# Performance work log

Hardware: AMD Instinct MI355X
Metric: run time of the kernel (lower is better)

The kernel has to match this reference:

```python
import jax, jax.numpy as jnp
import numpy as np

B, S, D = 2, 2048, 2048
H, KV, HD = 32, 8, 64  # num_heads, num_kv_heads, head_dim
NREP = H // KV


def rotate_half(x):
    x1, x2 = x[..., : x.shape[-1] // 2], x[..., x.shape[-1] // 2 :]
    return jnp.concatenate((-x2, x1), axis=-1)


def setup_inputs() -> dict:
    key = jax.random.key(0)
    ks = jax.random.split(key, 5)
    x = jax.random.normal(ks[0], (B, S, D), dtype=jnp.float32)
    # weights stored as [in, out] so y = x @ W (same math as nn.Linear with random init)
    Wq = jax.random.normal(ks[1], (D, D), dtype=jnp.float32) * (D ** -0.5)
    Wk = jax.random.normal(ks[2], (D, KV * HD), dtype=jnp.float32) * (D ** -0.5)
    Wv = jax.random.normal(ks[3], (D, KV * HD), dtype=jnp.float32) * (D ** -0.5)
    Wo = jax.random.normal(ks[4], (D, D), dtype=jnp.float32) * (D ** -0.5)
    # standard RoPE tables, broadcastable over [B, H, S, HD]
    inv_freq = 1.0 / (10000.0 ** (jnp.arange(0, HD, 2, dtype=jnp.float32) / HD))
    freqs = jnp.arange(S, dtype=jnp.float32)[:, None] * inv_freq[None, :]  # [S, HD/2]
    emb = jnp.concatenate((freqs, freqs), axis=-1)  # [S, HD]
    cos = jnp.cos(emb)[None, None]  # [1,1,S,HD]
    sin = jnp.sin(emb)[None, None]
    # causal mask, masked where == 0
    attention_mask = jnp.tril(jnp.ones((S, S), dtype=jnp.int32))[None, None]
    return {"x": x, "cos": cos, "sin": sin, "Wq": Wq, "Wk": Wk, "Wv": Wv,
            "Wo": Wo, "attention_mask": attention_mask}


def reference(x, cos, sin, Wq, Wk, Wv, Wo, attention_mask):
    b, s, _ = x.shape
    q = (x @ Wq).reshape(b, s, H, HD).transpose(0, 2, 1, 3)   # [B,H,S,HD]
    k = (x @ Wk).reshape(b, s, KV, HD).transpose(0, 2, 1, 3)  # [B,KV,S,HD]
    v = (x @ Wv).reshape(b, s, KV, HD).transpose(0, 2, 1, 3)  # [B,KV,S,HD]
    # RoPE (elementwise) commutes with head-repeat; apply before grouping
    q = q * cos + rotate_half(q) * sin
    k = k * cos + rotate_half(k) * sin
    # GQA head broadcast instead of repeat_interleave: group q as [B,KV,NREP,S,HD]
    qg = q.reshape(b, KV, NREP, s, HD)
    scores = jnp.einsum('bgrqd,bgkd->bgrqk', qg, k) / jnp.sqrt(jnp.float32(HD))
    scores = jnp.where(attention_mask[:, :, None] == 0, jnp.float32(-1e9), scores)
    probs = jax.nn.softmax(scores, axis=-1)
    out = jnp.einsum('bgrqk,bgkd->bgrqd', probs, v)           # [B,KV,NREP,S,HD]
    out = out.reshape(b, H, s, HD).transpose(0, 2, 1, 3).reshape(b, s, H * HD)
    return out @ Wo
```

## Files before the change

### kernel.cpp

```cpp
#include <hip/hip_runtime.h>
#include <hip/hip_bf16.h>
#include <stdint.h>

#define B_ 2
#define S_ 2048
#define D_ 2048
#define H_ 32
#define KV_ 8
#define HD_ 64
#define NQKV 3072

typedef __bf16 bf16_t;
typedef __bf16 bf16x8 __attribute__((ext_vector_type(8)));
typedef __bf16 bf16x4 __attribute__((ext_vector_type(4)));
typedef float  f32x4  __attribute__((ext_vector_type(4)));
typedef float  f32x16 __attribute__((ext_vector_type(16)));
typedef unsigned int u32;
typedef u32 u32x4 __attribute__((ext_vector_type(4)));

typedef const __attribute__((address_space(1))) uint32_t* gp1_t;
typedef __attribute__((address_space(3))) uint32_t* lp3_t;

__device__ inline void gload_lds16(const void* g, void* l) {
  __builtin_amdgcn_global_load_lds((gp1_t)(uintptr_t)g, (lp3_t)(uint32_t)(uintptr_t)l,
                                   16, 0, 0);
}

__device__ inline u32 pkbf(float a, float b) {
  union { bf16_t h[2]; u32 u; } v;
  v.h[0] = (bf16_t)a; v.h[1] = (bf16_t)b;
  return v.u;
}

__device__ inline void pl32swap(u32 &a, u32 &b) {
  asm("v_permlane32_swap_b32 %0, %1" : "+v"(a), "+v"(b));
}

__global__ void prep_all(const float* __restrict__ x, bf16_t* __restrict__ xb,
                         const float* __restrict__ Wq, const float* __restrict__ Wk,
                         const float* __restrict__ Wv, const float* __restrict__ Wo,
                         bf16_t* __restrict__ Wqkvt, bf16_t* __restrict__ Wot) {
  const int id = blockIdx.x;
  const int tid = threadIdx.y * 32 + threadIdx.x;
  if (id < 8192) {
    const int i = id * 256 + tid;
    float4 v = ((const float4*)x)[i];
    bf16x4 o;
    o[0] = (bf16_t)v.x; o[1] = (bf16_t)v.y; o[2] = (bf16_t)v.z; o[3] = (bf16_t)v.w;
    ((bf16x4*)xb)[i] = o;
    return;
  }
  __shared__ float t[32][33];
  const int wid = id - 8192;
  const float* in; bf16_t* out; int C, roff, bx, by;
  if (wid < 4096)      { in = Wq; out = Wqkvt; C = 2048; roff = 0;    bx = wid & 63;          by = wid >> 6; }
  else if (wid < 5120) { in = Wk; out = Wqkvt; C = 512;  roff = 2048; bx = (wid - 4096) & 15; by = (wid - 4096) >> 4; }
  else if (wid < 6144) { in = Wv; out = Wqkvt; C = 512;  roff = 2560; bx = (wid - 5120) & 15; by = (wid - 5120) >> 4; }
  else                 { in = Wo; out = Wot;   C = 2048; roff = 0;    bx = (wid - 6144) & 63; by = (wid - 6144) >> 6; }
  const int tx = threadIdx.x, ty = threadIdx.y;
  const int c0 = bx * 32, r0 = by * 32;
#pragma unroll
  for (int j = 0; j < 4; ++j)
    t[ty + j*8][tx] = in[(int64_t)(r0 + ty + j*8) * C + c0 + tx];
  __syncthreads();
#pragma unroll
  for (int j = 0; j < 4; ++j)
    out[(int64_t)(roff + c0 + ty + j*8) * 2048 + r0 + tx] = (bf16_t)t[tx][ty + j*8];
}

__global__ void v_transpose(const bf16_t* __restrict__ qkv, bf16_t* __restrict__ Vt) {
  __shared__ bf16_t t[32][34];
  const int tx = threadIdx.x, ty = threadIdx.y;
  const int c0 = blockIdx.x * 32;
  const int s0 = blockIdx.y * 32;
  const int b  = blockIdx.z;
#pragma unroll
  for (int j = 0; j < 4; ++j)
    t[ty + j*8][tx] = qkv[(int64_t)(b * S_ + s0 + ty + j*8) * NQKV + 2560 + c0 + tx];
  __syncthreads();
#pragma unroll
  for (int j = 0; j < 4; ++j)
    Vt[(int64_t)(b * 512 + c0 + ty + j*8) * S_ + s0 + tx] = t[tx][ty + j*8];
}

#define QSCALE 0.18033688011112042f
__global__ __launch_bounds__(256) void rope_scatter2(const bf16_t* __restrict__ qkv,
                                                     const float* __restrict__ cosb,
                                                     const float* __restrict__ sinb,
                                                     bf16_t* __restrict__ Q,
                                                     bf16_t* __restrict__ Kr) {
  const int row = blockIdx.x;
  const int b = row >> 11, s = row & 2047;
  const bf16_t* src = qkv + (int64_t)row * NQKV;
  const float* cs = cosb + s * HD_;
  const float* sn = sinb + s * HD_;
  const int tid = threadIdx.x;
  {
    const int c0 = tid * 8;
    const int d0 = c0 & 63, h = c0 >> 6;
    bf16x8 own = *(const bf16x8*)(src + c0);
    bf16x8 par = *(const bf16x8*)(src + (c0 ^ 32));
    const float sgn = (d0 & 32) ? 1.f : -1.f;
    bf16x8 o;
#pragma unroll
    for (int j = 0; j < 8; ++j) {
      const int d = d0 + j;
      float val = (float)own[j] * cs[d] + sgn * (float)par[j] * sn[d];
      o[j] = (bf16_t)(val * QSCALE);
    }
    *(bf16x8*)(Q + ((int64_t)(b * H_ + h) * S_ + s) * HD_ + d0) = o;
  }
  if (tid < 64) {
    const int c0 = 2048 + tid * 8;
    const int d0 = (tid * 8) & 63, kvh = tid >> 3;
    bf16x8 own = *(const bf16x8*)(src + c0);
    bf16x8 par = *(const bf16x8*)(src + (c0 ^ 32));
    const float sgn = (d0 & 32) ? 1.f : -1.f;
    bf16x8 o;
#pragma unroll
    for (int j = 0; j < 8; ++j) {
      const int d = d0 + j;
      float val = (float)own[j] * cs[d] + sgn * (float)par[j] * sn[d];
      o[j] = (bf16_t)val;
    }
    *(bf16x8*)(Kr + ((int64_t)(b * KV_ + kvh) * S_ + s) * HD_ + d0) = o;
  }
}

template <int BN, int EPI, typename OutT>
__global__ __launch_bounds__(512, 2) void gemm256(const bf16_t* __restrict__ A,
                                                  const bf16_t* __restrict__ Bt,
                                                  OutT* __restrict__ Cout,
                                                  int N, int K) {
  constexpr int NB = BN / 64;
  constexpr int LT = 4 + NB;
  constexpr int WCOLS = BN / 4;
  constexpr int NF = WCOLS / 16;

  __shared__ bf16_t As[2][256 * 64];
  __shared__ bf16_t Bs[2][BN * 64];

  const int tid = threadIdx.x;
  const int w = tid >> 6, lane = tid & 63;
  const int l15 = lane & 15, l4 = lane >> 4;
  const int wr = w >> 2, wc = w & 3;

  const int nX = gridDim.x;
  const int lin = blockIdx.y * nX + blockIdx.x;
  const int cpx = (nX * gridDim.y) >> 3;
  const int swz = (lin & 7) * cpx + (lin >> 3);
  const int bm = (swz / nX) * 256, bn = (swz % nX) * BN;

  const int rw = w * 8 + (lane >> 3);
  const int srcg = ((lane & 7) ^ ((lane >> 3) & 7)) << 3;
  const bf16_t* PA[4];
  const bf16_t* PB[NB];
#pragma unroll
  for (int L = 0; L < 4; ++L)
    PA[L] = A + (int64_t)(bm + L * 64 + rw) * K + srcg;
#pragma unroll
  for (int L = 0; L < NB; ++L)
    PB[L] = Bt + (int64_t)(bn + L * 64 + rw) * K + srcg;

  const int NK = K >> 6;
  const int xr = l15 & 7;
  const int g0 = (l4 ^ xr) << 3;
  const int g1 = ((4 + l4) ^ xr) << 3;

  f32x4 acc[8][NF] = {};

  auto stage = [&](int s, int buf, int toff) {
    if (s < 4) gload_lds16(PA[s] + toff, &As[buf][s * 4096 + w * 512]);
    else       gload_lds16(PB[s - 4] + toff, &Bs[buf][(s - 4) * 4096 + w * 512]);
  };

#pragma unroll
  for (int s = 0; s < LT; ++s) stage(s, 0, 0);
  asm volatile("s_waitcnt vmcnt(0)" ::: "memory");
  __syncthreads();

  for (int t = 0; t < NK; ++t) {
    const int p = t & 1;
    const bool more = (t + 1) < NK;
    const int toff = (t + 1) << 6;
    const bf16_t* Ab = &As[p][0];
    const bf16_t* Bb = &Bs[p][0];

    bf16x8 ball[NF][2];
#pragma unroll
    for (int nn = 0; nn < NF; ++nn) {
      const int rb = wc * WCOLS + nn * 16 + l15;
      ball[nn][0] = *(const bf16x8*)(Bb + rb * 64 + g0);
      ball[nn][1] = *(const bf16x8*)(Bb + rb * 64 + g1);
    }

#pragma unroll
    for (int mh = 0; mh < 2; ++mh) {
      if (more) {
        const int sb = mh * (LT / 2);
        const int se = (mh == 0) ? (LT / 2) : LT;
#pragma unroll
        for (int s = sb; s < se; ++s) stage(s, p ^ 1, toff);
      }
      bf16x8 af[4][2];
#pragma unroll
      for (int mm = 0; mm < 4; ++mm) {
        const int ra = wr * 128 + (mh * 4 + mm) * 16 + l15;
        af[mm][0] = *(const bf16x8*)(Ab + ra * 64 + g0);
        af[mm][1] = *(const bf16x8*)(Ab + ra * 64 + g1);
      }
      __builtin_amdgcn_s_setprio(1);
#pragma unroll
      for (int mm = 0; mm < 4; ++mm)
#pragma unroll
        for (int nn = 0; nn < NF; ++nn) {
          acc[mh*4+mm][nn] = __builtin_amdgcn_mfma_f32_16x16x32_bf16(
              af[mm][0], ball[nn][0], acc[mh*4+mm][nn], 0, 0, 0);
          acc[mh*4+mm][nn] = __builtin_amdgcn_mfma_f32_16x16x32_bf16(
              af[mm][1], ball[nn][1], acc[mh*4+mm][nn], 0, 0, 0);
        }
      __builtin_amdgcn_s_setprio(0);
    }
    if (more) {
      asm volatile("s_waitcnt vmcnt(0)" ::: "memory");
      __syncthreads();
    }
  }

#pragma unroll
  for (int m = 0; m < 8; ++m) {
    const int row = bm + wr * 128 + m * 16 + l4 * 4;
#pragma unroll
    for (int n = 0; n < NF; ++n) {
      const int col = bn + wc * WCOLS + n * 16 + l15;
#pragma unroll
      for (int r = 0; r < 4; ++r)
        Cout[(int64_t)(row + r) * N + col] = (OutT)acc[m][n][r];
    }
  }
}

__global__ __launch_bounds__(512, 2) void gemm_out3(const bf16_t* __restrict__ A,
                                                    const bf16_t* __restrict__ Bt,
                                                    float* __restrict__ Cout,
                                                    int N, int K) {
  constexpr int BN = 128, NB = 2, LT = 6, WCOLS = 32, NF = 2;

  __shared__ bf16_t As[3][256 * 64];
  __shared__ bf16_t Bs[3][BN * 64];

  const int tid = threadIdx.x;
  const int w = tid >> 6, lane = tid & 63;
  const int l15 = lane & 15, l4 = lane >> 4;
  const int wr = w >> 2, wc = w & 3;

  const int nX = gridDim.x;
  const int lin = blockIdx.y * nX + blockIdx.x;
  const int cpx = (nX * gridDim.y) >> 3;
  const int swz = (lin & 7) * cpx + (lin >> 3);
  const int bm = (swz / nX) * 256, bn = (swz % nX) * BN;

  const int rw = w * 8 + (lane >> 3);
  const int srcg = ((lane & 7) ^ ((lane >> 3) & 7)) << 3;
  const bf16_t* PA[4];
  const bf16_t* PB[NB];
#pragma unroll
  for (int L = 0; L < 4; ++L)
    PA[L] = A + (int64_t)(bm + L * 64 + rw) * K + srcg;
#pragma unroll
  for (int L = 0; L < NB; ++L)
    PB[L] = Bt + (int64_t)(bn + L * 64 + rw) * K + srcg;

  const int NK = K >> 6;
  const int xr = l15 & 7;
  const int g0 = (l4 ^ xr) << 3;
  const int g1 = ((4 + l4) ^ xr) << 3;

  f32x4 acc[8][NF] = {};

  auto stage = [&](int tsrc, int buf) {
    const int tc = (tsrc < NK) ? tsrc : (NK - 1);
    const int toff = tc << 6;
#pragma unroll
    for (int s = 0; s < 4; ++s)
      gload_lds16(PA[s] + toff, &As[buf][s * 4096 + w * 512]);
#pragma unroll
    for (int s = 0; s < NB; ++s)
      gload_lds16(PB[s] + toff, &Bs[buf][s * 4096 + w * 512]);
  };

  stage(0, 0);
  stage(1, 1);

  for (int t = 0; t < NK; ++t) {
    asm volatile("s_waitcnt vmcnt(6)" ::: "memory");
    asm volatile("s_barrier" ::: "memory");
    stage(t + 2, (t + 2) % 3);
    const bf16_t* Ab = &As[t % 3][0];
    const bf16_t* Bb = &Bs[t % 3][0];

    bf16x8 ball[NF][2];
#pragma unroll
    for (int nn = 0; nn < NF; ++nn) {
      const int rb = wc * WCOLS + nn * 16 + l15;
      ball[nn][0] = *(const bf16x8*)(Bb + rb * 64 + g0);
      ball[nn][1] = *(const bf16x8*)(Bb + rb * 64 + g1);
    }
#pragma unroll
    for (int mh = 0; mh < 2; ++mh) {
      bf16x8 af[4][2];
#pragma unroll
      for (int mm = 0; mm < 4; ++mm) {
        const int ra = wr * 128 + (mh * 4 + mm) * 16 + l15;
        af[mm][0] = *(const bf16x8*)(Ab + ra * 64 + g0);
        af[mm][1] = *(const bf16x8*)(Ab + ra * 64 + g1);
      }
      __builtin_amdgcn_s_setprio(1);
#pragma unroll
      for (int mm = 0; mm < 4; ++mm)
#pragma unroll
        for (int nn = 0; nn < NF; ++nn) {
          acc[mh*4+mm][nn] = __builtin_amdgcn_mfma_f32_16x16x32_bf16(
              af[mm][0], ball[nn][0], acc[mh*4+mm][nn], 0, 0, 0);
          acc[mh*4+mm][nn] = __builtin_amdgcn_mfma_f32_16x16x32_bf16(
              af[mm][1], ball[nn][1], acc[mh*4+mm][nn], 0, 0, 0);
        }
      __builtin_amdgcn_s_setprio(0);
    }
  }
  asm volatile("s_waitcnt vmcnt(0)" ::: "memory");

#pragma unroll
  for (int m = 0; m < 8; ++m) {
    const int row = bm + wr * 128 + m * 16 + l4 * 4;
#pragma unroll
    for (int n = 0; n < NF; ++n) {
      const int col = bn + wc * WCOLS + n * 16 + l15;
#pragma unroll
      for (int r = 0; r < 4; ++r)
        Cout[(int64_t)(row + r) * N + col] = acc[m][n][r];
    }
  }
}

#define SHIFT_ 8.0f
__global__ __launch_bounds__(256, 2) void attn9(const bf16_t* __restrict__ Q,
                                                const bf16_t* __restrict__ Kr,
                                                const bf16_t* __restrict__ Vt,
                                                bf16_t* __restrict__ AO) {
  const int bk = blockIdx.x;
  const int b = bk >> 3, kvh = bk & 7;
  const int y = blockIdx.y;
  const int q0A = y * 32, q0B = (63 - y) * 32;
  const int tid = threadIdx.x;
  const int w = tid >> 6, lane = tid & 63;
  const int l31 = lane & 31, hi = lane >> 5;
  const int h = kvh * 4 + w;

  __shared__ __align__(16) bf16_t Ks[3][64 * 64];
  __shared__ __align__(16) bf16_t Vs[3][64 * 64];

  const bf16_t* Kg = Kr + (int64_t)(b * KV_ + kvh) * S_ * HD_;
  const bf16_t* Vg = Vt + (int64_t)(b * KV_ + kvh) * HD_ * S_;

  const int rL = (w << 3) + (lane >> 3);
  const int sgr = ((lane & 7) ^ (rL & 7)) << 3;
  const bf16_t* Ksrc = Kg + (int64_t)rL * HD_ + sgr;
  const bf16_t* Vsrc = Vg + (int64_t)rL * S_ + sgr;

  const int NT = (63 - y) / 2 + 1;

  auto stage = [&](int t) {
    const int tc = (t < NT) ? t : (NT - 1);
    char* Kd = (char*)Ks + (t % 3) * 8192 + w * 1024;
    char* Vd = (char*)Vs + (t % 3) * 8192 + w * 1024;
    gload_lds16(Ksrc + (int64_t)tc * 64 * HD_, Kd);
    gload_lds16(Ksrc + (int64_t)(tc * 64 + 32) * HD_, Kd + 4096);
    gload_lds16(Vsrc + tc * 64, Vd);
    gload_lds16(Vsrc + (int64_t)32 * S_ + tc * 64, Vd + 4096);
  };

  const bf16_t* QbA = Q + ((int64_t)(b * H_ + h) * S_ + q0A) * HD_;
  const bf16_t* QbB = Q + ((int64_t)(b * H_ + h) * S_ + q0B) * HD_;
  bf16x8 qfA[4], qfB[4];
#pragma unroll
  for (int ds = 0; ds < 4; ++ds) {
    qfA[ds] = *(const bf16x8*)(QbA + l31 * HD_ + ds * 16 + hi * 8);
    qfB[ds] = *(const bf16x8*)(QbB + l31 * HD_ + ds * 16 + hi * 8);
  }

  bf16x8 onesf;
#pragma unroll
  for (int i = 0; i < 8; ++i) onesf[i] = (bf16_t)1.0f;

  f32x16 aA0 = {}, aA1 = {}, aB0 = {}, aB1 = {};
  f32x16 lA = {}, lB = {};
  const int xorb = l31 & 7;

  const f32x16 sinit = {-SHIFT_, -SHIFT_, -SHIFT_, -SHIFT_,
                        -SHIFT_, -SHIFT_, -SHIFT_, -SHIFT_,
                        -SHIFT_, -SHIFT_, -SHIFT_, -SHIFT_,
                        -SHIFT_, -SHIFT_, -SHIFT_, -SHIFT_};

  auto softmax_pack = [&](const f32x16 &sacc, bool diag,
                          bf16x8 &pf0, bf16x8 &pf1) {
    float p[16];
#pragma unroll
    for (int r = 0; r < 16; ++r) {
      float sc = sacc[r];
      if (diag) {
        int kvpos = (r & 3) + 8 * (r >> 2) + 4 * hi;
        if (kvpos > l31) sc = -1e30f;
      }
      p[r] = __builtin_amdgcn_exp2f(sc);
    }
    u32 pk[8];
#pragma unroll
    for (int i = 0; i < 8; ++i) pk[i] = pkbf(p[2*i], p[2*i+1]);
    u32 a0 = pk[0], b0 = pk[2]; pl32swap(a0, b0);
    u32 a1 = pk[1], b1 = pk[3]; pl32swap(a1, b1);
    u32 a2 = pk[4], b2 = pk[6]; pl32swap(a2, b2);
    u32 a3 = pk[5], b3 = pk[7]; pl32swap(a3, b3);
    pf0 = __builtin_bit_cast(bf16x8, (u32x4){a0, a1, b0, b1});
    pf1 = __builtin_bit_cast(bf16x8, (u32x4){a2, a3, b2, b3});
  };

  stage(0);
  stage(1);

  for (int t = 0; t < NT; ++t) {
    asm volatile("s_waitcnt vmcnt(4) lgkmcnt(0)" ::: "memory");
    asm volatile("s_barrier" ::: "memory");
    stage(t + 2);
    const char* KsB = (const char*)Ks + (t % 3) * 8192;
    const char* VsB = (const char*)Vs + (t % 3) * 8192;
#pragma unroll
    for (int sub = 0; sub < 2; ++sub) {
      const int kvbase = t * 64 + sub * 32;
      if (kvbase <= q0B) {
        const bool actA = (kvbase <= q0A);
        const char* Kbase = KsB + (sub * 32 + l31) * 128;
        bf16x8 kf[4];
#pragma unroll
        for (int ds = 0; ds < 4; ++ds)
          kf[ds] = *(const bf16x8*)(Kbase + ((((ds << 1) + hi) ^ xorb) << 4));
        f32x16 sA = sinit, sB = sinit;
        __builtin_amdgcn_s_setprio(1);
#pragma unroll
        for (int ds = 0; ds < 4; ++ds)
          sB = __builtin_amdgcn_mfma_f32_32x32x16_bf16(kf[ds], qfB[ds], sB, 0, 0, 0);
        if (actA) {
#pragma unroll
          for (int ds = 0; ds < 4; ++ds)
            sA = __builtin_amdgcn_mfma_f32_32x32x16_bf16(kf[ds], qfA[ds], sA, 0, 0, 0);
        }
        __builtin_amdgcn_s_setprio(0);
        const char* Vb0 = VsB + l31 * 128;
        const char* Vb1 = VsB + (32 + l31) * 128;
        const int c0 = (sub << 2) + hi;
        const int c1 = c0 + 2;
        bf16x8 v00 = *(const bf16x8*)(Vb0 + ((c0 ^ xorb) << 4));
        bf16x8 v01 = *(const bf16x8*)(Vb0 + ((c1 ^ xorb) << 4));
        bf16x8 v10 = *(const bf16x8*)(Vb1 + ((c0 ^ xorb) << 4));
        bf16x8 v11 = *(const bf16x8*)(Vb1 + ((c1 ^ xorb) << 4));
        bf16x8 pB0, pB1;
        softmax_pack(sB, kvbase == q0B, pB0, pB1);
        __builtin_amdgcn_s_setprio(1);
        aB0 = __builtin_amdgcn_mfma_f32_32x32x16_bf16(v00, pB0, aB0, 0, 0, 0);
        aB1 = __builtin_amdgcn_mfma_f32_32x32x16_bf16(v10, pB0, aB1, 0, 0, 0);
        aB0 = __builtin_amdgcn_mfma_f32_32x32x16_bf16(v01, pB1, aB0, 0, 0, 0);
        aB1 = __builtin_amdgcn_mfma_f32_32x32x16_bf16(v11, pB1, aB1, 0, 0, 0);
        lB  = __builtin_amdgcn_mfma_f32_32x32x16_bf16(onesf, pB0, lB, 0, 0, 0);
        lB  = __builtin_amdgcn_mfma_f32_32x32x16_bf16(onesf, pB1, lB, 0, 0, 0);
        __builtin_amdgcn_s_setprio(0);
        if (actA) {
          bf16x8 pA0, pA1;
          softmax_pack(sA, kvbase == q0A, pA0, pA1);
          __builtin_amdgcn_s_setprio(1);
          aA0 = __builtin_amdgcn_mfma_f32_32x32x16_bf16(v00, pA0, aA0, 0, 0, 0);
          aA1 = __builtin_amdgcn_mfma_f32_32x32x16_bf16(v10, pA0, aA1, 0, 0, 0);
          aA0 = __builtin_amdgcn_mfma_f32_32x32x16_bf16(v01, pA1, aA0, 0, 0, 0);
          aA1 = __builtin_amdgcn_mfma_f32_32x32x16_bf16(v11, pA1, aA1, 0, 0, 0);
          lA  = __builtin_amdgcn_mfma_f32_32x32x16_bf16(onesf, pA0, lA, 0, 0, 0);
          lA  = __builtin_amdgcn_mfma_f32_32x32x16_bf16(onesf, pA1, lA, 0, 0, 0);
          __builtin_amdgcn_s_setprio(0);
        }
      }
    }
  }

  asm volatile("s_waitcnt vmcnt(0)" ::: "memory");

  auto epi = [&](const f32x16 &a0, const f32x16 &a1, float denom, int q0) {
    const float rl = 1.f / denom;
    const int64_t row = (int64_t)(b * S_ + q0 + l31);
#pragma unroll
    for (int dt = 0; dt < 2; ++dt) {
#pragma unroll
      for (int g = 0; g < 4; ++g) {
        bf16x4 ov;
#pragma unroll
        for (int j = 0; j < 4; ++j) {
          float val = (dt ? a1[4*g + j] : a0[4*g + j]) * rl;
          ov[j] = (bf16_t)val;
        }
        const int d0 = dt * 32 + g * 8 + hi * 4;
        *(bf16x4*)(AO + row * D_ + h * HD_ + d0) = ov;
      }
    }
  };
  epi(aA0, aA1, lA[0], q0A);
  epi(aB0, aB1, lB[0], q0B);
}

extern "C" void kernel_launch(void* const* d_in, const int* in_sizes, int n_in,
                              void* d_out, int out_size, void* d_ws, size_t ws_size,
                              hipStream_t stream) {
  const float* x    = (const float*)d_in[0];
  const float* cosb = (const float*)d_in[1];
  const float* sinb = (const float*)d_in[2];
  const float* Wq   = (const float*)d_in[3];
  const float* Wk   = (const float*)d_in[4];
  const float* Wv   = (const float*)d_in[5];
  const float* Wo   = (const float*)d_in[6];
  float* out = (float*)d_out;

  bf16_t* ws = (bf16_t*)d_ws;
  size_t o = 0;
  bf16_t* xb    = ws + o; o += (size_t)4096 * 2048;
  bf16_t* Wqkvt = ws + o; o += (size_t)3072 * 2048;
  bf16_t* Wot   = ws + o; o += (size_t)2048 * 2048;
  bf16_t* qkv   = ws + o; o += (size_t)4096 * 3072;
  bf16_t* Qr    = ws + o; o += (size_t)B_ * H_ * S_ * HD_;
  bf16_t* Krb   = ws + o; o += (size_t)B_ * KV_ * S_ * HD_;
  bf16_t* Vtb   = ws + o; o += (size_t)B_ * KV_ * S_ * HD_;
  bf16_t* AO    = ws + o; o += (size_t)4096 * 2048;

  prep_all<<<18432, dim3(32, 8), 0, stream>>>(x, xb, Wq, Wk, Wv, Wo, Wqkvt, Wot);
  gemm256<192, 2, bf16_t><<<dim3(3072/192, 4096/256), 512, 0, stream>>>(
      xb, Wqkvt, qkv, 3072, 2048);
  rope_scatter2<<<4096, 256, 0, stream>>>(qkv, cosb, sinb, Qr, Krb);
  v_transpose<<<dim3(16, 64, 2), dim3(32, 8), 0, stream>>>(qkv, Vtb);
  attn9<<<dim3(16, 32), 256, 0, stream>>>(Qr, Krb, Vtb, AO);
  gemm_out3<<<dim3(2048/128, 4096/256), 512, 0, stream>>>(AO, Wot, out, 2048, 2048);
}
```

Baseline: 173.4 us.

## Merge RoPE and V-transpose launches; interleave loads with MFMA in output GEMM

```diff
diff --git a/kernel.cpp b/kernel.cpp
--- a/kernel.cpp
+++ b/kernel.cpp
@@ -68,12 +68,59 @@
     out[(int64_t)(roff + c0 + ty + j*8) * 2048 + r0 + tx] = (bf16_t)t[tx][ty + j*8];
 }
 
-__global__ void v_transpose(const bf16_t* __restrict__ qkv, bf16_t* __restrict__ Vt) {
+#define QSCALE 0.18033688011112042f
+__global__ __launch_bounds__(256) void scatter_all(const bf16_t* __restrict__ qkv,
+                                                   const float* __restrict__ cosb,
+                                                   const float* __restrict__ sinb,
+                                                   bf16_t* __restrict__ Q,
+                                                   bf16_t* __restrict__ Kr,
+                                                   bf16_t* __restrict__ Vt) {
+  const int id = blockIdx.x;
+  const int tid = threadIdx.x;
+  if (id < 4096) {
+    const int row = id;
+    const int b = row >> 11, s = row & 2047;
+    const bf16_t* src = qkv + (int64_t)row * NQKV;
+    const float* cs = cosb + s * HD_;
+    const float* sn = sinb + s * HD_;
+    {
+      const int c0 = tid * 8;
+      const int d0 = c0 & 63, h = c0 >> 6;
+      bf16x8 own = *(const bf16x8*)(src + c0);
+      bf16x8 par = *(const bf16x8*)(src + (c0 ^ 32));
+      const float sgn = (d0 & 32) ? 1.f : -1.f;
+      bf16x8 o;
+#pragma unroll
+      for (int j = 0; j < 8; ++j) {
+        const int d = d0 + j;
+        float val = (float)own[j] * cs[d] + sgn * (float)par[j] * sn[d];
+        o[j] = (bf16_t)(val * QSCALE);
+      }
+      *(bf16x8*)(Q + ((int64_t)(b * H_ + h) * S_ + s) * HD_ + d0) = o;
+    }
+    if (tid < 64) {
+      const int c0 = 2048 + tid * 8;
+      const int d0 = (tid * 8) & 63, kvh = tid >> 3;
+      bf16x8 own = *(const bf16x8*)(src + c0);
+      bf16x8 par = *(const bf16x8*)(src + (c0 ^ 32));
+      const float sgn = (d0 & 32) ? 1.f : -1.f;
+      bf16x8 o;
+#pragma unroll
+      for (int j = 0; j < 8; ++j) {
+        const int d = d0 + j;
+        float val = (float)own[j] * cs[d] + sgn * (float)par[j] * sn[d];
+        o[j] = (bf16_t)val;
+      }
+      *(bf16x8*)(Kr + ((int64_t)(b * KV_ + kvh) * S_ + s) * HD_ + d0) = o;
+    }
+    return;
+  }
   __shared__ bf16_t t[32][34];
-  const int tx = threadIdx.x, ty = threadIdx.y;
-  const int c0 = blockIdx.x * 32;
-  const int s0 = blockIdx.y * 32;
-  const int b  = blockIdx.z;
+  const int wid = id - 4096;
+  const int c0 = (wid & 15) * 32;
+  const int s0 = ((wid >> 4) & 63) * 32;
+  const int b  = wid >> 10;
+  const int tx = tid & 31, ty = tid >> 5;
 #pragma unroll
   for (int j = 0; j < 4; ++j)
     t[ty + j*8][tx] = qkv[(int64_t)(b * S_ + s0 + ty + j*8) * NQKV + 2560 + c0 + tx];
@@ -81,50 +128,6 @@
 #pragma unroll
   for (int j = 0; j < 4; ++j)
     Vt[(int64_t)(b * 512 + c0 + ty + j*8) * S_ + s0 + tx] = t[tx][ty + j*8];
-}
-
-#define QSCALE 0.18033688011112042f
-__global__ __launch_bounds__(256) void rope_scatter2(const bf16_t* __restrict__ qkv,
-                                                     const float* __restrict__ cosb,
-                                                     const float* __restrict__ sinb,
-                                                     bf16_t* __restrict__ Q,
-                                                     bf16_t* __restrict__ Kr) {
-  const int row = blockIdx.x;
-  const int b = row >> 11, s = row & 2047;
-  const bf16_t* src = qkv + (int64_t)row * NQKV;
-  const float* cs = cosb + s * HD_;
-  const float* sn = sinb + s * HD_;
-  const int tid = threadIdx.x;
-  {
-    const int c0 = tid * 8;
-    const int d0 = c0 & 63, h = c0 >> 6;
-    bf16x8 own = *(const bf16x8*)(src + c0);
-    bf16x8 par = *(const bf16x8*)(src + (c0 ^ 32));
-    const float sgn = (d0 & 32) ? 1.f : -1.f;
-    bf16x8 o;
-#pragma unroll
-    for (int j = 0; j < 8; ++j) {
-      const int d = d0 + j;
-      float val = (float)own[j] * cs[d] + sgn * (float)par[j] * sn[d];
-      o[j] = (bf16_t)(val * QSCALE);
-    }
-    *(bf16x8*)(Q + ((int64_t)(b * H_ + h) * S_ + s) * HD_ + d0) = o;
-  }
-  if (tid < 64) {
-    const int c0 = 2048 + tid * 8;
-    const int d0 = (tid * 8) & 63, kvh = tid >> 3;
-    bf16x8 own = *(const bf16x8*)(src + c0);
-    bf16x8 par = *(const bf16x8*)(src + (c0 ^ 32));
-    const float sgn = (d0 & 32) ? 1.f : -1.f;
-    bf16x8 o;
-#pragma unroll
-    for (int j = 0; j < 8; ++j) {
-      const int d = d0 + j;
-      float val = (float)own[j] * cs[d] + sgn * (float)par[j] * sn[d];
-      o[j] = (bf16_t)val;
-    }
-    *(bf16x8*)(Kr + ((int64_t)(b * KV_ + kvh) * S_ + s) * HD_ + d0) = o;
-  }
 }
 
 template <int BN, int EPI, typename OutT>
@@ -240,14 +243,14 @@
   }
 }
 
-__global__ __launch_bounds__(512, 2) void gemm_out3(const bf16_t* __restrict__ A,
-                                                    const bf16_t* __restrict__ Bt,
-                                                    float* __restrict__ Cout,
-                                                    int N, int K) {
-  constexpr int BN = 128, NB = 2, LT = 6, WCOLS = 32, NF = 2;
+__global__ __launch_bounds__(512, 2) void gemm_out8p(const bf16_t* __restrict__ A,
+                                                     const bf16_t* __restrict__ Bt,
+                                                     float* __restrict__ Cout,
+                                                     int N, int K) {
+  constexpr int WCOLS = 32, NF = 2;
 
   __shared__ bf16_t As[3][256 * 64];
-  __shared__ bf16_t Bs[3][BN * 64];
+  __shared__ bf16_t Bs[3][128 * 64];
 
   const int tid = threadIdx.x;
   const int w = tid >> 6, lane = tid & 63;
@@ -258,17 +261,17 @@
   const int lin = blockIdx.y * nX + blockIdx.x;
   const int cpx = (nX * gridDim.y) >> 3;
   const int swz = (lin & 7) * cpx + (lin >> 3);
-  const int bm = (swz / nX) * 256, bn = (swz % nX) * BN;
+  const int bm = (swz / nX) * 256, bn = (swz % nX) * 128;
 
   const int rw = w * 8 + (lane >> 3);
   const int srcg = ((lane & 7) ^ ((lane >> 3) & 7)) << 3;
   const bf16_t* PA[4];
-  const bf16_t* PB[NB];
+  const bf16_t* PB[2];
 #pragma unroll
   for (int L = 0; L < 4; ++L)
     PA[L] = A + (int64_t)(bm + L * 64 + rw) * K + srcg;
 #pragma unroll
-  for (int L = 0; L < NB; ++L)
+  for (int L = 0; L < 2; ++L)
     PB[L] = Bt + (int64_t)(bn + L * 64 + rw) * K + srcg;
 
   const int NK = K >> 6;
@@ -278,55 +281,84 @@
 
   f32x4 acc[8][NF] = {};
 
-  auto stage = [&](int tsrc, int buf) {
+  auto stageu = [&](int tsrc, int buf, int u) {
     const int tc = (tsrc < NK) ? tsrc : (NK - 1);
     const int toff = tc << 6;
-#pragma unroll
-    for (int s = 0; s < 4; ++s)
-      gload_lds16(PA[s] + toff, &As[buf][s * 4096 + w * 512]);
-#pragma unroll
-    for (int s = 0; s < NB; ++s)
-      gload_lds16(PB[s] + toff, &Bs[buf][s * 4096 + w * 512]);
-  };
-
-  stage(0, 0);
-  stage(1, 1);
+    if (u < 2) {
+      gload_lds16(PA[2*u]     + toff, &As[buf][(2*u)     * 4096 + w * 512]);
+      gload_lds16(PA[2*u + 1] + toff, &As[buf][(2*u + 1) * 4096 + w * 512]);
+    } else {
+      gload_lds16(PB[0] + toff, &Bs[buf][w * 512]);
+      gload_lds16(PB[1] + toff, &Bs[buf][4096 + w * 512]);
+    }
+  };
+  auto readA = [&](bf16x8 (&af)[4][2], const bf16_t* Ab, int mh) {
+#pragma unroll
+    for (int mm = 0; mm < 4; ++mm) {
+      const int ra = wr * 128 + (mh * 4 + mm) * 16 + l15;
+      af[mm][0] = *(const bf16x8*)(Ab + ra * 64 + g0);
+      af[mm][1] = *(const bf16x8*)(Ab + ra * 64 + g1);
+    }
+  };
+  auto readB = [&](bf16x8 (&bf)[2], const bf16_t* Bb, int nf) {
+    const int rb = wc * WCOLS + nf * 16 + l15;
+    bf[0] = *(const bf16x8*)(Bb + rb * 64 + g0);
+    bf[1] = *(const bf16x8*)(Bb + rb * 64 + g1);
+  };
+  auto mfma8 = [&](bf16x8 (&af)[4][2], bf16x8 (&bf)[2], int mh, int nf) {
+    __builtin_amdgcn_s_setprio(1);
+#pragma unroll
+    for (int mm = 0; mm < 4; ++mm) {
+      acc[mh*4+mm][nf] = __builtin_amdgcn_mfma_f32_16x16x32_bf16(
+          af[mm][0], bf[0], acc[mh*4+mm][nf], 0, 0, 0);
+      acc[mh*4+mm][nf] = __builtin_amdgcn_mfma_f32_16x16x32_bf16(
+          af[mm][1], bf[1], acc[mh*4+mm][nf], 0, 0, 0);
+    }
+    __builtin_amdgcn_s_setprio(0);
+  };
+  auto wait_lds = [&]() {
+    asm volatile("s_waitcnt lgkmcnt(0)" ::: "memory");
+    __builtin_amdgcn_sched_barrier(0);
+  };
+
+#pragma unroll
+  for (int u = 0; u < 3; ++u) stageu(0, 0, u);
+#pragma unroll
+  for (int u = 0; u < 3; ++u) stageu(1, 1, u);
+  asm volatile("s_waitcnt vmcnt(6)" ::: "memory");
+  asm volatile("s_barrier" ::: "memory");
 
   for (int t = 0; t < NK; ++t) {
+    const int cb = t % 3, nb = (t + 2) % 3;
+    const bf16_t* Ab = &As[cb][0];
+    const bf16_t* Bb = &Bs[cb][0];
+    bf16x8 aH[4][2], bf0[2], bf1[2];
+
+    readA(aH, Ab, 0);
+    readB(bf0, Bb, 0);
+    stageu(t + 2, nb, 0);
+    asm volatile("s_barrier" ::: "memory");
+    wait_lds();
+    mfma8(aH, bf0, 0, 0);
+    asm volatile("s_barrier" ::: "memory");
+
+    readB(bf1, Bb, 1);
+    stageu(t + 2, nb, 1);
+    asm volatile("s_barrier" ::: "memory");
+    wait_lds();
+    mfma8(aH, bf1, 0, 1);
+    asm volatile("s_barrier" ::: "memory");
+
+    readA(aH, Ab, 1);
+    stageu(t + 2, nb, 2);
+    asm volatile("s_barrier" ::: "memory");
+    wait_lds();
+    mfma8(aH, bf1, 1, 1);
+    asm volatile("s_barrier" ::: "memory");
+
+    mfma8(aH, bf0, 1, 0);
     asm volatile("s_waitcnt vmcnt(6)" ::: "memory");
     asm volatile("s_barrier" ::: "memory");
-    stage(t + 2, (t + 2) % 3);
-    const bf16_t* Ab = &As[t % 3][0];
-    const bf16_t* Bb = &Bs[t % 3][0];
-
-    bf16x8 ball[NF][2];
-#pragma unroll
-    for (int nn = 0; nn < NF; ++nn) {
-      const int rb = wc * WCOLS + nn * 16 + l15;
-      ball[nn][0] = *(const bf16x8*)(Bb + rb * 64 + g0);
-      ball[nn][1] = *(const bf16x8*)(Bb + rb * 64 + g1);
-    }
-#pragma unroll
-    for (int mh = 0; mh < 2; ++mh) {
-      bf16x8 af[4][2];
-#pragma unroll
-      for (int mm = 0; mm < 4; ++mm) {
-        const int ra = wr * 128 + (mh * 4 + mm) * 16 + l15;
-        af[mm][0] = *(const bf16x8*)(Ab + ra * 64 + g0);
-        af[mm][1] = *(const bf16x8*)(Ab + ra * 64 + g1);
-      }
-      __builtin_amdgcn_s_setprio(1);
-#pragma unroll
-      for (int mm = 0; mm < 4; ++mm)
-#pragma unroll
-        for (int nn = 0; nn < NF; ++nn) {
-          acc[mh*4+mm][nn] = __builtin_amdgcn_mfma_f32_16x16x32_bf16(
-              af[mm][0], ball[nn][0], acc[mh*4+mm][nn], 0, 0, 0);
-          acc[mh*4+mm][nn] = __builtin_amdgcn_mfma_f32_16x16x32_bf16(
-              af[mm][1], ball[nn][1], acc[mh*4+mm][nn], 0, 0, 0);
-        }
-      __builtin_amdgcn_s_setprio(0);
-    }
   }
   asm volatile("s_waitcnt vmcnt(0)" ::: "memory");
 
@@ -539,8 +571,7 @@
   prep_all<<<18432, dim3(32, 8), 0, stream>>>(x, xb, Wq, Wk, Wv, Wo, Wqkvt, Wot);
   gemm256<192, 2, bf16_t><<<dim3(3072/192, 4096/256), 512, 0, stream>>>(
       xb, Wqkvt, qkv, 3072, 2048);
-  rope_scatter2<<<4096, 256, 0, stream>>>(qkv, cosb, sinb, Qr, Krb);
-  v_transpose<<<dim3(16, 64, 2), dim3(32, 8), 0, stream>>>(qkv, Vtb);
+  scatter_all<<<6144, 256, 0, stream>>>(qkv, cosb, sinb, Qr, Krb, Vtb);
   attn9<<<dim3(16, 32), 256, 0, stream>>>(Qr, Krb, Vtb, AO);
-  gemm_out3<<<dim3(2048/128, 4096/256), 512, 0, stream>>>(AO, Wot, out, 2048, 2048);
-}
+  gemm_out8p<<<dim3(2048/128, 4096/256), 512, 0, stream>>>(AO, Wot, out, 2048, 2048);
+}
```

Result: no change. 173.4 us (-0.0%).
